# Kernel optimization log

Hardware: AMD Instinct MI355X
Metric: run time of the kernel (lower is better)

The kernel has to match this reference:

```python
import jax, jax.numpy as jnp
import numpy as np

DIM = 768
HEADS = 12
HEAD_DIM = DIM // HEADS
HIDDEN = int(DIM * 4.0)
EPS = 1e-5


def _layernorm(x, g, b):
    mu = jnp.mean(x, axis=-1, keepdims=True)
    var = jnp.var(x, axis=-1, keepdims=True)
    return (x - mu) * jax.lax.rsqrt(var + EPS) * g + b


def setup_inputs() -> dict:
    key = jax.random.key(0)
    ks = jax.random.split(key, 12)
    s = 0.02
    return {
        "x": jax.random.normal(ks[0], (8, 1024, DIM), dtype=jnp.float32),
        "norm1_g": jnp.ones((DIM,), jnp.float32),
        "norm1_b": jnp.zeros((DIM,), jnp.float32),
        "qkv_w": jax.random.normal(ks[1], (3 * DIM, DIM), jnp.float32) * s,
        "qkv_b": jnp.zeros((3 * DIM,), jnp.float32),
        "proj_w": jax.random.normal(ks[2], (DIM, DIM), jnp.float32) * s,
        "proj_b": jnp.zeros((DIM,), jnp.float32),
        "norm2_g": jnp.ones((DIM,), jnp.float32),
        "norm2_b": jnp.zeros((DIM,), jnp.float32),
        "fc1_w": jax.random.normal(ks[3], (HIDDEN, DIM), jnp.float32) * s,
        "fc1_b": jnp.zeros((HIDDEN,), jnp.float32),
        "fc2_w": jax.random.normal(ks[4], (DIM, HIDDEN), jnp.float32) * s,
        "fc2_b": jnp.zeros((DIM,), jnp.float32),
    }


def reference(x, norm1_g, norm1_b, qkv_w, qkv_b, proj_w, proj_b,
              norm2_g, norm2_b, fc1_w, fc1_b, fc2_w, fc2_b):
    B, N, C = x.shape
    scale = HEAD_DIM ** -0.5

    # --- MHSA with pre-norm + residual ---
    h = _layernorm(x, norm1_g, norm1_b)
    qkv = h @ qkv_w.T + qkv_b                      # [B, N, 3C]
    qkv = qkv.reshape(B, N, 3, HEADS, HEAD_DIM)
    qkv = jnp.transpose(qkv, (2, 0, 3, 1, 4))      # [3, B, H, N, Dh]
    q, k, v = qkv[0], qkv[1], qkv[2]
    attn = jnp.einsum("bhnd,bhmd->bhnm", q, k) * scale
    attn = jax.nn.softmax(attn, axis=-1)
    o = jnp.einsum("bhnm,bhmd->bhnd", attn, v)     # [B, H, N, Dh]
    o = jnp.transpose(o, (0, 2, 1, 3)).reshape(B, N, C)
    x = x + (o @ proj_w.T + proj_b)

    # --- MLP with pre-norm + residual ---
    h = _layernorm(x, norm2_g, norm2_b)
    h = jax.nn.gelu(h @ fc1_w.T + fc1_b, approximate=False)
    x = x + (h @ fc2_w.T + fc2_b)
    return x
```

## Files before the change

### kernel.cpp

```cpp
#include <hip/hip_runtime.h>
#include <hip/hip_bf16.h>

typedef unsigned short u16;
using short8  = __attribute__((ext_vector_type(8))) short;
using floatx4 = __attribute__((ext_vector_type(4))) float;

__device__ inline u16 f2bu(float f) {
    __hip_bfloat16 h = __float2bfloat16(f);
    return __builtin_bit_cast(u16, h);
}
__device__ inline float b2f(u16 u) {
    unsigned v = (unsigned)u << 16;
    return __builtin_bit_cast(float, v);
}

__device__ inline void load16(const u16* g, u16* l) {
    __builtin_amdgcn_global_load_lds(
        (const __attribute__((address_space(1))) void*)g,
        (__attribute__((address_space(3))) void*)l, 16, 0, 0);
}

__global__ void cvt_bf16v(const float4* __restrict__ in, ushort4* __restrict__ out, int n4) {
    int i = blockIdx.x * 256 + threadIdx.x;
    if (i < n4) {
        float4 f = in[i];
        ushort4 r;
        r.x = f2bu(f.x); r.y = f2bu(f.y); r.z = f2bu(f.z); r.w = f2bu(f.w);
        out[i] = r;
    }
}

__global__ __launch_bounds__(256) void layernorm_bf16(
    const float* __restrict__ x, const float* __restrict__ g,
    const float* __restrict__ b, u16* __restrict__ out)
{
    int row = blockIdx.x;
    int tid = threadIdx.x;
    const float* xr = x + (size_t)row * 768;
    float v0 = xr[tid], v1 = xr[tid + 256], v2 = xr[tid + 512];
    float s = v0 + v1 + v2;
    float ss = v0 * v0 + v1 * v1 + v2 * v2;
    for (int off = 1; off < 64; off <<= 1) {
        s  += __shfl_xor(s, off, 64);
        ss += __shfl_xor(ss, off, 64);
    }
    __shared__ float as[4], ass[4];
    int wave = tid >> 6, lane = tid & 63;
    if (lane == 0) { as[wave] = s; ass[wave] = ss; }
    __syncthreads();
    s  = as[0] + as[1] + as[2] + as[3];
    ss = ass[0] + ass[1] + ass[2] + ass[3];
    float mu  = s * (1.0f / 768.0f);
    float var = ss * (1.0f / 768.0f) - mu * mu;
    float rs  = rsqrtf(var + 1e-5f);
    u16* orow = out + (size_t)row * 768;
    orow[tid]       = f2bu((v0 - mu) * rs * g[tid]       + b[tid]);
    orow[tid + 256] = f2bu((v1 - mu) * rs * g[tid + 256] + b[tid + 256]);
    orow[tid + 512] = f2bu((v2 - mu) * rs * g[tid + 512] + b[tid + 512]);
}

__global__ __launch_bounds__(256) void fc2_reduce(
    const ushort4* __restrict__ P0, const ushort4* __restrict__ P1,
    const float* __restrict__ bias, float4* __restrict__ out)
{
    int i = blockIdx.x * 256 + threadIdx.x;
    int col = (i % 192) * 4;
    ushort4 a = P0[i], b = P1[i];
    float4 o = out[i];
    o.x += bias[col + 0] + b2f(a.x) + b2f(b.x);
    o.y += bias[col + 1] + b2f(a.y) + b2f(b.y);
    o.z += bias[col + 2] + b2f(a.z) + b2f(b.z);
    o.w += bias[col + 3] + b2f(a.w) + b2f(b.w);
    out[i] = o;
}

__global__ __launch_bounds__(256) void gemm_bt(
    const u16* __restrict__ A, int lda,
    const u16* __restrict__ B, int ldb,
    int K,
    const float* __restrict__ bias,
    const float* __restrict__ res,
    float* __restrict__ outf, u16* __restrict__ outb, u16* __restrict__ outb2,
    int ldc, int act, int splits)
{
    __shared__ u16 lsa[2 * 128 * 32];
    __shared__ u16 lsb[2 * 128 * 32];

    int tid  = threadIdx.x;
    int wave = tid >> 6, lane = tid & 63;
    int quad = lane >> 4, l16 = lane & 15;
    int wrow = (wave >> 1) * 64;
    int wcol = (wave & 1) * 64;

    int gx = gridDim.x;
    int nblk = gx * gridDim.y;
    int flat = blockIdx.y * gx + blockIdx.x;
    int d = (flat & 7) * (nblk >> 3) + (flat >> 3);
    int m0 = (d / gx) * 128, n0 = (d % gx) * 128;

    int Kper = K / splits;
    int kbeg = blockIdx.z * Kper;
    int nIter = Kper >> 5;

    floatx4 acc[4][4];
    for (int i = 0; i < 4; ++i)
        for (int j = 0; j < 4; ++j)
            acc[i][j] = (floatx4){0.f, 0.f, 0.f, 0.f};

    int srow = wave * 32 + (lane >> 2);
    int scol = (((lane & 3) ^ ((lane >> 3) & 3))) * 8;
    const u16* ga0 = A + (size_t)(m0 + srow)      * lda + kbeg + scol;
    const u16* ga1 = A + (size_t)(m0 + srow + 16) * lda + kbeg + scol;
    const u16* gb0 = B + (size_t)(n0 + srow)      * ldb + kbeg + scol;
    const u16* gb1 = B + (size_t)(n0 + srow + 16) * ldb + kbeg + scol;
    int lofs = wave * 1024;

    int xq = (quad ^ ((l16 >> 1) & 3)) * 8;

    load16(ga0, &lsa[lofs]);
    load16(ga1, &lsa[lofs + 512]);
    load16(gb0, &lsb[lofs]);
    load16(gb1, &lsb[lofs + 512]);
    ga0 += 32; ga1 += 32; gb0 += 32; gb1 += 32;

    for (int it = 0; it < nIter; ++it) {
        int cur = (it & 1) * 4096;
        __syncthreads();
        if (it + 1 < nIter) {
            int nxt = cur ^ 4096;
            load16(ga0, &lsa[nxt + lofs]);
            load16(ga1, &lsa[nxt + lofs + 512]);
            load16(gb0, &lsb[nxt + lofs]);
            load16(gb1, &lsb[nxt + lofs + 512]);
            ga0 += 32; ga1 += 32; gb0 += 32; gb1 += 32;
        }
        short8 af[4], bfr[4];
        #pragma unroll
        for (int rb = 0; rb < 4; ++rb) af[rb]  = *(short8*)&lsa[cur + (wrow + rb * 16 + l16) * 32 + xq];
        #pragma unroll
        for (int cb = 0; cb < 4; ++cb) bfr[cb] = *(short8*)&lsb[cur + (wcol + cb * 16 + l16) * 32 + xq];
        #pragma unroll
        for (int rb = 0; rb < 4; ++rb)
            #pragma unroll
            for (int cb = 0; cb < 4; ++cb)
                acc[rb][cb] = __builtin_amdgcn_mfma_f32_16x16x32_bf16(af[rb], bfr[cb], acc[rb][cb], 0, 0, 0);
    }

    u16* pdst = (splits > 1) ? (blockIdx.z ? outb2 : outb) : outb;
    #pragma unroll
    for (int rb = 0; rb < 4; ++rb)
        #pragma unroll
        for (int cb = 0; cb < 4; ++cb)
            #pragma unroll
            for (int r = 0; r < 4; ++r) {
                int row = m0 + wrow + rb * 16 + quad * 4 + r;
                int col = n0 + wcol + cb * 16 + l16;
                float v = acc[rb][cb][r];
                if (splits > 1) {
                    pdst[(size_t)row * ldc + col] = f2bu(v);
                } else {
                    v += bias[col];
                    if (res) v += res[(size_t)row * ldc + col];
                    if (act) v = 0.5f * v * (1.0f + erff(v * 0.70710678118654752f));
                    if (outf) outf[(size_t)row * ldc + col] = v;
                    else      pdst[(size_t)row * ldc + col] = f2bu(v);
                }
            }
}

__global__ __launch_bounds__(256) void attn_fused(
    const u16* __restrict__ qkv, u16* __restrict__ o)
{
    const int N = 1024, C3 = 2304;
    int qb = blockIdx.x;
    int bh = blockIdx.y;
    int b = bh / 12, h = bh % 12;
    int tid = threadIdx.x, wave = tid >> 6, lane = tid & 63;
    int quad = lane >> 4, l16 = lane & 15;

    __shared__ u16 lk[64 * 64];
    __shared__ u16 lvt[64][72];
    __shared__ u16 lp[4][16][72];

    const size_t base = (size_t)b * N * C3;
    int q0 = qb * 64 + wave * 16;

    short8 qa0 = *(const short8*)&qkv[base + (size_t)(q0 + l16) * C3 + h * 64 + quad * 8];
    short8 qa1 = *(const short8*)&qkv[base + (size_t)(q0 + l16) * C3 + h * 64 + 32 + quad * 8];

    floatx4 oacc[4];
    for (int i = 0; i < 4; ++i) oacc[i] = (floatx4){0.f, 0.f, 0.f, 0.f};
    float lsum[4] = {0.f, 0.f, 0.f, 0.f};

    for (int kt = 0; kt < N; kt += 64) {
        __syncthreads();
        #pragma unroll
        for (int i = 0; i < 2; ++i) {
            int idx = i * 2048 + wave * 512 + lane * 8;
            int r = idx >> 6;
            int gc = (lane & 7) ^ (r & 7);
            load16(&qkv[base + (size_t)(kt + r) * C3 + 768 + h * 64 + gc * 8], &lk[idx]);
        }
        {
            int key = tid & 63, dbase = (tid >> 6) * 16;
            const u16* vp = &qkv[base + (size_t)(kt + key) * C3 + 1536 + h * 64 + dbase];
            uint4 vv0 = *(const uint4*)vp;
            uint4 vv1 = *(const uint4*)(vp + 8);
            const u16* e0 = (const u16*)&vv0;
            const u16* e1 = (const u16*)&vv1;
            #pragma unroll
            for (int i = 0; i < 8; ++i) {
                lvt[dbase + i][key]     = e0[i];
                lvt[dbase + 8 + i][key] = e1[i];
            }
        }
        __syncthreads();

        float p[4][4];
        #pragma unroll
        for (int kb = 0; kb < 4; ++kb) {
            int R = kb * 16 + l16;
            short8 b0 = *(short8*)&lk[R * 64 + ((quad ^ (R & 7)) * 8)];
            short8 b1 = *(short8*)&lk[R * 64 + (((quad + 4) ^ (R & 7)) * 8)];
            floatx4 c = (floatx4){0.f, 0.f, 0.f, 0.f};
            c = __builtin_amdgcn_mfma_f32_16x16x32_bf16(qa0, b0, c, 0, 0, 0);
            c = __builtin_amdgcn_mfma_f32_16x16x32_bf16(qa1, b1, c, 0, 0, 0);
            #pragma unroll
            for (int r = 0; r < 4; ++r) {
                p[kb][r] = __expf(c[r] * 0.125f);
                lsum[r] += p[kb][r];
            }
        }
        #pragma unroll
        for (int kb = 0; kb < 4; ++kb)
            #pragma unroll
            for (int r = 0; r < 4; ++r)
                lp[wave][quad * 4 + r][kb * 16 + l16] = f2bu(p[kb][r]);

        short8 pa0 = *(short8*)&lp[wave][l16][quad * 8];
        short8 pa1 = *(short8*)&lp[wave][l16][32 + quad * 8];
        #pragma unroll
        for (int db = 0; db < 4; ++db) {
            short8 vb0 = *(short8*)&lvt[db * 16 + l16][quad * 8];
            short8 vb1 = *(short8*)&lvt[db * 16 + l16][32 + quad * 8];
            oacc[db] = __builtin_amdgcn_mfma_f32_16x16x32_bf16(pa0, vb0, oacc[db], 0, 0, 0);
            oacc[db] = __builtin_amdgcn_mfma_f32_16x16x32_bf16(pa1, vb1, oacc[db], 0, 0, 0);
        }
    }

    #pragma unroll
    for (int r = 0; r < 4; ++r)
        for (int off = 1; off < 16; off <<= 1)
            lsum[r] += __shfl_xor(lsum[r], off, 64);

    #pragma unroll
    for (int db = 0; db < 4; ++db)
        #pragma unroll
        for (int r = 0; r < 4; ++r) {
            int row = q0 + quad * 4 + r;
            int col = h * 64 + db * 16 + l16;
            o[(size_t)(b * N + row) * 768 + col] = f2bu(oacc[db][r] / lsum[r]);
        }
}

extern "C" void kernel_launch(void* const* d_in, const int* in_sizes, int n_in,
                              void* d_out, int out_size, void* d_ws, size_t ws_size,
                              hipStream_t stream) {
    const float* x      = (const float*)d_in[0];
    const float* n1g    = (const float*)d_in[1];
    const float* n1b    = (const float*)d_in[2];
    const float* qkv_w  = (const float*)d_in[3];
    const float* qkv_b  = (const float*)d_in[4];
    const float* proj_w = (const float*)d_in[5];
    const float* proj_b = (const float*)d_in[6];
    const float* n2g    = (const float*)d_in[7];
    const float* n2b    = (const float*)d_in[8];
    const float* fc1_w  = (const float*)d_in[9];
    const float* fc1_b  = (const float*)d_in[10];
    const float* fc2_w  = (const float*)d_in[11];
    const float* fc2_b  = (const float*)d_in[12];
    float* out = (float*)d_out;

    const int T = 8192;
    char* ws = (char*)d_ws;
    u16* w_qkv  = (u16*)ws;               ws += (size_t)2304 * 768 * 2;
    u16* w_proj = (u16*)ws;               ws += (size_t)768 * 768 * 2;
    u16* w_fc1  = (u16*)ws;               ws += (size_t)3072 * 768 * 2;
    u16* w_fc2  = (u16*)ws;               ws += (size_t)768 * 3072 * 2;
    u16* h_buf  = (u16*)ws;               ws += (size_t)T * 768 * 2;
    u16* qkvbuf = (u16*)ws;               ws += (size_t)T * 2304 * 2;
    u16* o_buf  = (u16*)ws;               ws += (size_t)T * 768 * 2;
    u16* fc1out = qkvbuf;

    cvt_bf16v<<<dim3(2304 * 768 / 4 / 256), 256, 0, stream>>>((const float4*)qkv_w,  (ushort4*)w_qkv,  2304 * 768 / 4);
    cvt_bf16v<<<dim3(768 * 768 / 4 / 256),  256, 0, stream>>>((const float4*)proj_w, (ushort4*)w_proj, 768 * 768 / 4);
    cvt_bf16v<<<dim3(3072 * 768 / 4 / 256), 256, 0, stream>>>((const float4*)fc1_w,  (ushort4*)w_fc1,  3072 * 768 / 4);
    cvt_bf16v<<<dim3(768 * 3072 / 4 / 256), 256, 0, stream>>>((const float4*)fc2_w,  (ushort4*)w_fc2,  768 * 3072 / 4);

    layernorm_bf16<<<dim3(T), 256, 0, stream>>>(x, n1g, n1b, h_buf);
    gemm_bt<<<dim3(2304 / 128, T / 128), 256, 0, stream>>>(
        h_buf, 768, w_qkv, 768, 768, qkv_b, nullptr, nullptr, qkvbuf, nullptr, 2304, 0, 1);
    attn_fused<<<dim3(16, 96), 256, 0, stream>>>(qkvbuf, o_buf);
    gemm_bt<<<dim3(768 / 128, T / 128), 256, 0, stream>>>(
        o_buf, 768, w_proj, 768, 768, proj_b, x, out, nullptr, nullptr, 768, 0, 1);
    layernorm_bf16<<<dim3(T), 256, 0, stream>>>(out, n2g, n2b, h_buf);
    gemm_bt<<<dim3(3072 / 128, T / 128), 256, 0, stream>>>(
        h_buf, 768, w_fc1, 768, 768, fc1_b, nullptr, nullptr, fc1out, nullptr, 3072, 1, 1);
    gemm_bt<<<dim3(768 / 128, T / 128, 2), 256, 0, stream>>>(
        fc1out, 3072, w_fc2, 3072, 3072, fc2_b, nullptr, nullptr, h_buf, o_buf, 768, 0, 2);
    fc2_reduce<<<dim3(T * 768 / 4 / 256), 256, 0, stream>>>(
        (const ushort4*)h_buf, (const ushort4*)o_buf, fc2_b, (float4*)out);
}
```

Before: 451.1 us.

## Add 256x128 GEMM tile for QKV/FC1, split-K proj, tanh GELU

```diff
diff --git a/kernel.cpp b/kernel.cpp
--- a/kernel.cpp
+++ b/kernel.cpp
@@ -12,6 +12,10 @@
 __device__ inline float b2f(u16 u) {
     unsigned v = (unsigned)u << 16;
     return __builtin_bit_cast(float, v);
+}
+__device__ inline float gelu_f(float v) {
+    float u = 1.5957691216f * (v + 0.044715f * v * v * v);
+    return v / (1.f + __expf(-u));
 }
 
 __device__ inline void load16(const u16* g, u16* l) {
@@ -59,19 +63,101 @@
     orow[tid + 512] = f2bu((v2 - mu) * rs * g[tid + 512] + b[tid + 512]);
 }
 
-__global__ __launch_bounds__(256) void fc2_reduce(
+__global__ __launch_bounds__(256) void red2(
     const ushort4* __restrict__ P0, const ushort4* __restrict__ P1,
-    const float* __restrict__ bias, float4* __restrict__ out)
+    const float* __restrict__ bias, const float4* __restrict__ res,
+    float4* __restrict__ out)
 {
     int i = blockIdx.x * 256 + threadIdx.x;
     int col = (i % 192) * 4;
     ushort4 a = P0[i], b = P1[i];
-    float4 o = out[i];
+    float4 o = res ? res[i] : out[i];
     o.x += bias[col + 0] + b2f(a.x) + b2f(b.x);
     o.y += bias[col + 1] + b2f(a.y) + b2f(b.y);
     o.z += bias[col + 2] + b2f(a.z) + b2f(b.z);
     o.w += bias[col + 3] + b2f(a.w) + b2f(b.w);
     out[i] = o;
+}
+
+__global__ __launch_bounds__(256) void gemm_bt256(
+    const u16* __restrict__ A, int lda,
+    const u16* __restrict__ B, int ldb,
+    int K,
+    const float* __restrict__ bias,
+    u16* __restrict__ outb, int ldc, int act)
+{
+    __shared__ u16 lsa[2 * 256 * 32];
+    __shared__ u16 lsb[2 * 128 * 32];
+
+    int tid  = threadIdx.x;
+    int wave = tid >> 6, lane = tid & 63;
+    int quad = lane >> 4, l16 = lane & 15;
+
+    int gx = gridDim.x;
+    int nblk = gx * gridDim.y;
+    int flat = blockIdx.y * gx + blockIdx.x;
+    int d = (flat & 7) * (nblk >> 3) + (flat >> 3);
+    int m0 = (d / gx) * 256, n0 = (d % gx) * 128;
+
+    int nIter = K >> 5;
+
+    floatx4 acc[4][8];
+    for (int i = 0; i < 4; ++i)
+        for (int j = 0; j < 8; ++j)
+            acc[i][j] = (floatx4){0.f, 0.f, 0.f, 0.f};
+
+    int lrow = lane >> 2;
+    int scol = (((lane & 3) ^ ((lane >> 3) & 3))) * 8;
+    const u16* ga[4];
+    #pragma unroll
+    for (int j = 0; j < 4; ++j)
+        ga[j] = A + (size_t)(m0 + wave * 64 + j * 16 + lrow) * lda + scol;
+    const u16* gb[2];
+    #pragma unroll
+    for (int j = 0; j < 2; ++j)
+        gb[j] = B + (size_t)(n0 + wave * 32 + j * 16 + lrow) * ldb + scol;
+
+    int xq = (quad ^ ((l16 >> 1) & 3)) * 8;
+
+    #pragma unroll
+    for (int j = 0; j < 4; ++j) { load16(ga[j], &lsa[wave * 2048 + j * 512]); ga[j] += 32; }
+    #pragma unroll
+    for (int j = 0; j < 2; ++j) { load16(gb[j], &lsb[wave * 1024 + j * 512]); gb[j] += 32; }
+
+    for (int it = 0; it < nIter; ++it) {
+        int curA = (it & 1) * 8192, curB = (it & 1) * 4096;
+        __syncthreads();
+        if (it + 1 < nIter) {
+            int nA = curA ^ 8192, nB = curB ^ 4096;
+            #pragma unroll
+            for (int j = 0; j < 4; ++j) { load16(ga[j], &lsa[nA + wave * 2048 + j * 512]); ga[j] += 32; }
+            #pragma unroll
+            for (int j = 0; j < 2; ++j) { load16(gb[j], &lsb[nB + wave * 1024 + j * 512]); gb[j] += 32; }
+        }
+        short8 af[4], bfr[8];
+        #pragma unroll
+        for (int rb = 0; rb < 4; ++rb) af[rb]  = *(short8*)&lsa[curA + (wave * 64 + rb * 16 + l16) * 32 + xq];
+        #pragma unroll
+        for (int cb = 0; cb < 8; ++cb) bfr[cb] = *(short8*)&lsb[curB + (cb * 16 + l16) * 32 + xq];
+        #pragma unroll
+        for (int rb = 0; rb < 4; ++rb)
+            #pragma unroll
+            for (int cb = 0; cb < 8; ++cb)
+                acc[rb][cb] = __builtin_amdgcn_mfma_f32_16x16x32_bf16(af[rb], bfr[cb], acc[rb][cb], 0, 0, 0);
+    }
+
+    #pragma unroll
+    for (int rb = 0; rb < 4; ++rb)
+        #pragma unroll
+        for (int cb = 0; cb < 8; ++cb)
+            #pragma unroll
+            for (int r = 0; r < 4; ++r) {
+                int row = m0 + wave * 64 + rb * 16 + quad * 4 + r;
+                int col = n0 + cb * 16 + l16;
+                float v = acc[rb][cb][r] + bias[col];
+                if (act) v = gelu_f(v);
+                outb[(size_t)row * ldc + col] = f2bu(v);
+            }
 }
 
 __global__ __launch_bounds__(256) void gemm_bt(
@@ -80,7 +166,8 @@
     int K,
     const float* __restrict__ bias,
     const float* __restrict__ res,
-    float* __restrict__ outf, u16* __restrict__ outb, u16* __restrict__ outb2,
+    float* __restrict__ outf, u16* __restrict__ outb,
+    u16* __restrict__ parts, size_t pstride,
     int ldc, int act, int splits)
 {
     __shared__ u16 lsa[2 * 128 * 32];
@@ -146,7 +233,7 @@
                 acc[rb][cb] = __builtin_amdgcn_mfma_f32_16x16x32_bf16(af[rb], bfr[cb], acc[rb][cb], 0, 0, 0);
     }
 
-    u16* pdst = (splits > 1) ? (blockIdx.z ? outb2 : outb) : outb;
+    u16* pdst = (splits > 1) ? parts + (size_t)blockIdx.z * pstride : nullptr;
     #pragma unroll
     for (int rb = 0; rb < 4; ++rb)
         #pragma unroll
@@ -161,9 +248,9 @@
                 } else {
                     v += bias[col];
                     if (res) v += res[(size_t)row * ldc + col];
-                    if (act) v = 0.5f * v * (1.0f + erff(v * 0.70710678118654752f));
+                    if (act) v = gelu_f(v);
                     if (outf) outf[(size_t)row * ldc + col] = v;
-                    else      pdst[(size_t)row * ldc + col] = f2bu(v);
+                    else      outb[(size_t)row * ldc + col] = f2bu(v);
                 }
             }
 }
@@ -290,7 +377,10 @@
     u16* h_buf  = (u16*)ws;               ws += (size_t)T * 768 * 2;
     u16* qkvbuf = (u16*)ws;               ws += (size_t)T * 2304 * 2;
     u16* o_buf  = (u16*)ws;               ws += (size_t)T * 768 * 2;
+    u16* pbuf   = (u16*)ws;               ws += (size_t)T * 768 * 2;
     u16* fc1out = qkvbuf;
+    bool do_split = (size_t)(ws - (char*)d_ws) <= ws_size;
+    size_t pstr = (size_t)(pbuf - h_buf);
 
     cvt_bf16v<<<dim3(2304 * 768 / 4 / 256), 256, 0, stream>>>((const float4*)qkv_w,  (ushort4*)w_qkv,  2304 * 768 / 4);
     cvt_bf16v<<<dim3(768 * 768 / 4 / 256),  256, 0, stream>>>((const float4*)proj_w, (ushort4*)w_proj, 768 * 768 / 4);
@@ -298,16 +388,30 @@
     cvt_bf16v<<<dim3(768 * 3072 / 4 / 256), 256, 0, stream>>>((const float4*)fc2_w,  (ushort4*)w_fc2,  768 * 3072 / 4);
 
     layernorm_bf16<<<dim3(T), 256, 0, stream>>>(x, n1g, n1b, h_buf);
-    gemm_bt<<<dim3(2304 / 128, T / 128), 256, 0, stream>>>(
-        h_buf, 768, w_qkv, 768, 768, qkv_b, nullptr, nullptr, qkvbuf, nullptr, 2304, 0, 1);
+    gemm_bt256<<<dim3(2304 / 128, T / 256), 256, 0, stream>>>(
+        h_buf, 768, w_qkv, 768, 768, qkv_b, qkvbuf, 2304, 0);
     attn_fused<<<dim3(16, 96), 256, 0, stream>>>(qkvbuf, o_buf);
-    gemm_bt<<<dim3(768 / 128, T / 128), 256, 0, stream>>>(
-        o_buf, 768, w_proj, 768, 768, proj_b, x, out, nullptr, nullptr, 768, 0, 1);
+    if (do_split) {
+        gemm_bt<<<dim3(768 / 128, T / 128, 2), 256, 0, stream>>>(
+            o_buf, 768, w_proj, 768, 768, proj_b, nullptr, nullptr, nullptr,
+            h_buf, pstr, 768, 0, 2);
+        red2<<<dim3(T * 768 / 4 / 256), 256, 0, stream>>>(
+            (const ushort4*)h_buf, (const ushort4*)pbuf, proj_b, (const float4*)x, (float4*)out);
+    } else {
+        gemm_bt<<<dim3(768 / 128, T / 128), 256, 0, stream>>>(
+            o_buf, 768, w_proj, 768, 768, proj_b, x, out, nullptr, nullptr, 0, 768, 0, 1);
+    }
     layernorm_bf16<<<dim3(T), 256, 0, stream>>>(out, n2g, n2b, h_buf);
-    gemm_bt<<<dim3(3072 / 128, T / 128), 256, 0, stream>>>(
-        h_buf, 768, w_fc1, 768, 768, fc1_b, nullptr, nullptr, fc1out, nullptr, 3072, 1, 1);
-    gemm_bt<<<dim3(768 / 128, T / 128, 2), 256, 0, stream>>>(
-        fc1out, 3072, w_fc2, 3072, 3072, fc2_b, nullptr, nullptr, h_buf, o_buf, 768, 0, 2);
-    fc2_reduce<<<dim3(T * 768 / 4 / 256), 256, 0, stream>>>(
-        (const ushort4*)h_buf, (const ushort4*)o_buf, fc2_b, (float4*)out);
-}
+    gemm_bt256<<<dim3(3072 / 128, T / 256), 256, 0, stream>>>(
+        h_buf, 768, w_fc1, 768, 768, fc1_b, fc1out, 3072, 1);
+    if (do_split) {
+        gemm_bt<<<dim3(768 / 128, T / 128, 2), 256, 0, stream>>>(
+            fc1out, 3072, w_fc2, 3072, 3072, fc2_b, nullptr, nullptr, nullptr,
+            h_buf, pstr, 768, 0, 2);
+        red2<<<dim3(T * 768 / 4 / 256), 256, 0, stream>>>(
+            (const ushort4*)h_buf, (const ushort4*)pbuf, fc2_b, nullptr, (float4*)out);
+    } else {
+        gemm_bt<<<dim3(768 / 128, T / 128), 256, 0, stream>>>(
+            fc1out, 3072, w_fc2, 3072, 3072, fc2_b, out, out, nullptr, nullptr, 0, 768, 0, 1);
+    }
+}
```

Result: no change. 454.5 us (+0.8%).
